# Kernel optimization log

Measured on AMD Instinct MI355X. Metric: run time of the kernel, lower is better.

The kernel has to match this reference:

```python
import jax, jax.numpy as jnp
import numpy as np
from jax import lax

B, N, D = 2, 2048, 1024
H = 16
DH = D // H
EXP = 4
INNER = EXP * D
KS = 3
POWER = 2
LN_EPS = 1e-5


def _layer_norm(x, g, b):
    mu = jnp.mean(x, axis=-1, keepdims=True)
    var = jnp.mean(jnp.square(x - mu), axis=-1, keepdims=True)
    return (x - mu) * lax.rsqrt(var + LN_EPS) * g + b


def setup_inputs() -> dict:
    key = jax.random.key(0)
    ks = jax.random.split(key, 12)
    s = 1.0 / np.sqrt(D)
    si = 1.0 / np.sqrt(INNER)
    return {
        "Q_in": jax.random.normal(ks[0], (B, N, D), jnp.float32),
        "X": jax.random.normal(ks[1], (B, N, D), jnp.float32),
        "Wq": jax.random.normal(ks[2], (D, D), jnp.float32) * s,
        "Wk": jax.random.normal(ks[3], (D, D), jnp.float32) * s,
        "Wv": jax.random.normal(ks[4], (D, D), jnp.float32) * s,
        "Wo": jax.random.normal(ks[5], (D, D), jnp.float32) * s,
        "Wup": jax.random.normal(ks[6], (D, 2 * INNER), jnp.float32) * s,
        "conv_w": jax.random.normal(ks[7], (INNER, 1, KS), jnp.float32) * 0.5,
        "Wdown": jax.random.normal(ks[8], (INNER, D), jnp.float32) * si,
        "g1": jnp.ones((D,), jnp.float32),
        "b1": jnp.zeros((D,), jnp.float32),
        "g2": jnp.ones((D,), jnp.float32),
        "b2": jnp.zeros((D,), jnp.float32),
        "dt": jnp.float32(0.1),
    }


def reference(Q_in, X, Wq, Wk, Wv, Wo, Wup, conv_w, Wdown, g1, b1, g2, b2, dt):
    Bn, Nn, d = Q_in.shape
    # --- attention path: kernelized quadratic attention (relu^power) ---
    Hc = _layer_norm(Q_in, g1, b1) + X                     # [B,N,d]
    def heads(x):
        return x.reshape(Bn, Nn, H, DH).transpose(0, 2, 1, 3)  # [B,H,N,dh]
    Qp = heads(Hc @ Wq)
    Kp = heads(Hc @ Wk)
    Vp = heads(Hc @ Wv)
    PhiQ = jax.nn.elu(Qp) + 1.0
    PhiK = jax.nn.elu(Kp) + 1.0
    W = jnp.einsum("bhnd,bhmd->bhnm", PhiQ, PhiK)          # [B,H,N,N]
    W = jnp.maximum(W, 0.0) ** POWER
    Attr = jnp.einsum("bhnm,bhmd->bhnd", W, Vp)
    Norm = jnp.sum(W, axis=-1, keepdims=True) + 1.0
    m = Attr / Norm - Vp                                   # [B,H,N,dh]
    m_concat = m.transpose(0, 2, 1, 3).reshape(Bn, Nn, d)
    dt_safe = jax.nn.softplus(dt)
    Q_interact = Q_in + dt_safe * (m_concat @ Wo)
    # --- gated depthwise-conv FFN (ConvSwiGLU) ---
    Qn2 = _layer_norm(Q_interact, g2, b2)
    GU = Qn2 @ Wup                                         # [B,N,2*INNER]
    G, U = GU[..., :INNER], GU[..., INNER:]
    Hf = jax.nn.silu(G) * U                                # [B,N,INNER]
    Hf_t = Hf.transpose(0, 2, 1)                           # [B,INNER,N]
    pad = (KS - 1) // 2
    Hc_t = lax.conv_general_dilated(
        Hf_t, conv_w, window_strides=(1,), padding=[(pad, pad)],
        dimension_numbers=("NCH", "OIH", "NCH"), feature_group_count=INNER)
    H_out = Hc_t.transpose(0, 2, 1) @ Wdown
    return Q_interact + H_out
```

## Files before the change

### kernel.cpp

```cpp
#include <hip/hip_runtime.h>

typedef unsigned short u16;
typedef __attribute__((ext_vector_type(8))) __bf16 bf16x8;
typedef __attribute__((ext_vector_type(4))) float f32x4;
typedef __attribute__((ext_vector_type(8))) unsigned short us8v;

__device__ __forceinline__ u16 f2bf(float x){
  union { float f; unsigned u; } v; v.f = x;
  unsigned r = v.u + 0x7fffu + ((v.u >> 16) & 1u);
  return (u16)(r >> 16);
}
__device__ __forceinline__ float bf2f(u16 h){
  union { unsigned u; float f; } v; v.u = ((unsigned)h) << 16;
  return v.f;
}
__device__ __forceinline__ void gld16(const void* g, void* l){
  __builtin_amdgcn_global_load_lds((const __attribute__((address_space(1))) unsigned int*)g,
                                   (__attribute__((address_space(3))) unsigned int*)l, 16, 0, 0);
}

__global__ __launch_bounds__(256) void tr_all(
    const float* __restrict__ Wq, const float* __restrict__ Wk,
    const float* __restrict__ Wv, const float* __restrict__ Wo,
    const float* __restrict__ Wup, const float* __restrict__ Wdown,
    u16* __restrict__ WqkvT, u16* __restrict__ WoT,
    u16* __restrict__ WupT, u16* __restrict__ WdT)
{
  __shared__ float t[32][33];
  int tx = threadIdx.x, ty = threadIdx.y;
  int id = blockIdx.x;
  if (id < 4096){
    int w = id >> 10, b = id & 1023;
    int c0 = (b & 31)*32, r0 = (b >> 5)*32;
    const float* S = (w==0)?Wq:(w==1)?Wk:(w==2)?Wv:Wo;
    u16* D = (w==3)? WoT : (WqkvT + (size_t)w*1024*1024);
    #pragma unroll
    for (int j=0;j<32;j+=8) t[ty+j][tx] = S[(size_t)(r0+ty+j)*1024 + (c0+tx)];
    __syncthreads();
    #pragma unroll
    for (int j=0;j<32;j+=8) D[(size_t)(c0+ty+j)*1024 + (r0+tx)] = f2bf(t[tx][ty+j]);
  } else if (id < 12288){
    int b = id - 4096;
    int c0 = (b & 255)*32, r0 = (b >> 8)*32;
    #pragma unroll
    for (int j=0;j<32;j+=8) t[ty+j][tx] = Wup[(size_t)(r0+ty+j)*8192 + (c0+tx)];
    __syncthreads();
    #pragma unroll
    for (int j=0;j<32;j+=8){
      int c = c0 + ty + j;
      int rdst = (c < 4096) ? ((c>>4)*32 + (c&15)) : (((c-4096)>>4)*32 + 16 + (c&15));
      WupT[(size_t)rdst*1024 + (r0+tx)] = f2bf(t[tx][ty+j]);
    }
  } else {
    int b = id - 12288;
    int c0 = (b & 31)*32, r0 = (b >> 5)*32;
    #pragma unroll
    for (int j=0;j<32;j+=8) t[ty+j][tx] = Wdown[(size_t)(r0+ty+j)*1024 + (c0+tx)];
    __syncthreads();
    #pragma unroll
    for (int j=0;j<32;j+=8) WdT[(size_t)(c0+ty+j)*4096 + (r0+tx)] = f2bf(t[tx][ty+j]);
  }
}

__global__ __launch_bounds__(256) void ln_kernel(const float* __restrict__ Q, const float* __restrict__ X,
    const float* __restrict__ g, const float* __restrict__ b, u16* __restrict__ O){
  int row = blockIdx.x, tid = threadIdx.x;
  const float4 x = ((const float4*)(Q + (size_t)row*1024))[tid];
  float s = x.x + x.y + x.z + x.w;
  float sq = x.x*x.x + x.y*x.y + x.z*x.z + x.w*x.w;
  #pragma unroll
  for (int o=32;o>0;o>>=1){ s += __shfl_xor(s, o); sq += __shfl_xor(sq, o); }
  __shared__ float ss[4], ssq[4];
  int wid = tid>>6;
  if ((tid&63)==0){ ss[wid]=s; ssq[wid]=sq; }
  __syncthreads();
  s = ss[0]+ss[1]+ss[2]+ss[3]; sq = ssq[0]+ssq[1]+ssq[2]+ssq[3];
  float mu = s*(1.0f/1024.0f);
  float var = sq*(1.0f/1024.0f) - mu*mu;
  float rstd = rsqrtf(var + 1e-5f);
  float4 xx = make_float4(0.f,0.f,0.f,0.f);
  if (X) xx = ((const float4*)(X + (size_t)row*1024))[tid];
  float4 gv = ((const float4*)g)[tid];
  float4 bv = ((const float4*)b)[tid];
  ushort4 o;
  o.x = f2bf((x.x-mu)*rstd*gv.x + bv.x + xx.x);
  o.y = f2bf((x.y-mu)*rstd*gv.y + bv.y + xx.y);
  o.z = f2bf((x.z-mu)*rstd*gv.z + bv.z + xx.z);
  o.w = f2bf((x.w-mu)*rstd*gv.w + bv.w + xx.w);
  ((ushort4*)(O + (size_t)row*1024))[tid] = o;
}

__global__ __launch_bounds__(256) void ln2_kernel(const float* __restrict__ P,
    const float* __restrict__ Qin, const float* __restrict__ dtp,
    const float* __restrict__ g, const float* __restrict__ b,
    float* __restrict__ Qint, u16* __restrict__ Qn2){
  int row = blockIdx.x, tid = threadIdx.x;
  float sp = log1pf(__expf(dtp[0]));
  size_t off = (size_t)row*1024;
  float4 p0 = ((const float4*)(P + off))[tid];
  float4 p1 = ((const float4*)(P + 4194304 + off))[tid];
  float4 q  = ((const float4*)(Qin + off))[tid];
  float4 x;
  x.x = q.x + sp*(p0.x+p1.x); x.y = q.y + sp*(p0.y+p1.y);
  x.z = q.z + sp*(p0.z+p1.z); x.w = q.w + sp*(p0.w+p1.w);
  ((float4*)(Qint + off))[tid] = x;
  float s = x.x + x.y + x.z + x.w;
  float sq = x.x*x.x + x.y*x.y + x.z*x.z + x.w*x.w;
  #pragma unroll
  for (int o=32;o>0;o>>=1){ s += __shfl_xor(s, o); sq += __shfl_xor(sq, o); }
  __shared__ float ss[4], ssq[4];
  int wid = tid>>6;
  if ((tid&63)==0){ ss[wid]=s; ssq[wid]=sq; }
  __syncthreads();
  s = ss[0]+ss[1]+ss[2]+ss[3]; sq = ssq[0]+ssq[1]+ssq[2]+ssq[3];
  float mu = s*(1.0f/1024.0f);
  float var = sq*(1.0f/1024.0f) - mu*mu;
  float rstd = rsqrtf(var + 1e-5f);
  float4 gv = ((const float4*)g)[tid];
  float4 bv = ((const float4*)b)[tid];
  ushort4 o;
  o.x = f2bf((x.x-mu)*rstd*gv.x + bv.x);
  o.y = f2bf((x.y-mu)*rstd*gv.y + bv.y);
  o.z = f2bf((x.z-mu)*rstd*gv.z + bv.z);
  o.w = f2bf((x.w-mu)*rstd*gv.w + bv.w);
  ((ushort4*)(Qn2 + off))[tid] = o;
}

__global__ __launch_bounds__(256, 3) void gemm_qkv(
    const u16* __restrict__ A, const u16* __restrict__ Bt, void* __restrict__ Op)
{
  __shared__ u16 As[128*32];
  __shared__ u16 Bs[128*32];
  const int tid = threadIdx.x, wid = tid>>6, lane = tid&63;
  const int g = lane>>4, l = lane&15;
  const int row0 = blockIdx.x*128, col0 = blockIdx.y*128;
  const int wr = (wid&1)*64, wc = (wid>>1)*64;
  const int l3 = l & 3;
  f32x4 acc[4][4] = {};
  for (int k0 = 0; k0 < 1024; k0 += 32){
    __syncthreads();
    #pragma unroll
    for (int i=0;i<2;i++){
      int ch0 = i*256 + wid*64;
      int ch = ch0 + lane;
      int r = ch >> 2, c = ch & 3;
      int cs = c ^ (r & 3);
      gld16(A  + (size_t)(row0+r)*1024 + k0 + cs*8, (char*)As + ch0*16);
      gld16(Bt + (size_t)(col0+r)*1024 + k0 + cs*8, (char*)Bs + ch0*16);
    }
    __syncthreads();
    bf16x8 a[4], b[4];
    #pragma unroll
    for (int i=0;i<4;i++) a[i] = *(const bf16x8*)(As + (wr + i*16 + l)*32 + (g^l3)*8);
    #pragma unroll
    for (int j=0;j<4;j++) b[j] = *(const bf16x8*)(Bs + (wc + j*16 + l)*32 + (g^l3)*8);
    #pragma unroll
    for (int i=0;i<4;i++)
      #pragma unroll
      for (int j=0;j<4;j++)
        acc[i][j] = __builtin_amdgcn_mfma_f32_16x16x32_bf16(a[i], b[j], acc[i][j], 0, 0, 0);
  }
  u16* P = (u16*)Op;
  #pragma unroll
  for (int i=0;i<4;i++)
   #pragma unroll
   for (int j=0;j<4;j++){
     int col = col0 + wc + j*16 + l;
     int qk = col >> 10, c = col & 1023;
     int h = c >> 6, d = c & 63;
     int rowb = row0 + wr + i*16 + g*4;
     int bb = rowb >> 11, n = rowb & 2047;
     if (qk == 2){
       ushort4 vs;
       vs.x = f2bf(acc[i][j][0]); vs.y = f2bf(acc[i][j][1]);
       vs.z = f2bf(acc[i][j][2]); vs.w = f2bf(acc[i][j][3]);
       *(ushort4*)(P + (size_t)8388608 + (((size_t)(bb*16 + h))*64 + d)*2048 + n) = vs;
     } else {
       #pragma unroll
       for (int r=0;r<4;r++){
         float v = acc[i][j][r];
         float phi = v > 0.f ? v + 1.f : __expf(v);
         P[(size_t)qk*4194304 + (((size_t)(bb*16 + h))*2048 + (n+r))*64 + d] = f2bf(phi);
       }
     }
   }
}

__global__ __launch_bounds__(256, 2) void gemm_wide_up(
    const u16* __restrict__ A, const u16* __restrict__ Bt, u16* __restrict__ Op)
{
  __shared__ u16 As[256*32];
  __shared__ u16 Bs[128*32];
  const int tid = threadIdx.x, wid = tid>>6, lane = tid&63;
  const int g = lane>>4, l = lane&15, l3 = l&3;
  const int bid = blockIdx.x;
  const int bx = bid & 15;
  const int by = (bid>>7)*8 + ((bid>>4) & 7);
  const int row0 = bx*256, col0 = by*128;
  const int wr = (wid&1)*128, wc = (wid>>1)*64;
  f32x4 acc[8][4] = {};
  for (int k0 = 0; k0 < 1024; k0 += 32){
    __syncthreads();
    #pragma unroll
    for (int i=0;i<4;i++){
      int ch0 = i*256 + wid*64;
      int ch = ch0 + lane;
      int r = ch >> 2, c = ch & 3;
      int cs = c ^ (r & 3);
      gld16(A + (size_t)(row0+r)*1024 + k0 + cs*8, (char*)As + ch0*16);
    }
    #pragma unroll
    for (int i=0;i<2;i++){
      int ch0 = i*256 + wid*64;
      int ch = ch0 + lane;
      int r = ch >> 2, c = ch & 3;
      int cs = c ^ (r & 3);
      gld16(Bt + (size_t)(col0+r)*1024 + k0 + cs*8, (char*)Bs + ch0*16);
    }
    __syncthreads();
    bf16x8 a[8], b[4];
    #pragma unroll
    for (int i=0;i<8;i++) a[i] = *(const bf16x8*)(As + (wr + i*16 + l)*32 + (g^l3)*8);
    #pragma unroll
    for (int j=0;j<4;j++) b[j] = *(const bf16x8*)(Bs + (wc + j*16 + l)*32 + (g^l3)*8);
    #pragma unroll
    for (int i=0;i<8;i++)
      #pragma unroll
      for (int j=0;j<4;j++)
        acc[i][j] = __builtin_amdgcn_mfma_f32_16x16x32_bf16(a[i], b[j], acc[i][j], 0, 0, 0);
  }
  #pragma unroll
  for (int i=0;i<8;i++)
   #pragma unroll
   for (int jj=0;jj<4;jj+=2)
    #pragma unroll
    for (int r=0;r<4;r++){
      int row = row0 + wr + i*16 + g*4 + r;
      int pair = (col0 + wc + jj*16) >> 5;
      float G = acc[i][jj][r], U = acc[i][jj+1][r];
      float hf = G/(1.f+__expf(-G))*U;
      Op[(size_t)row*4096 + pair*16 + l] = f2bf(hf);
    }
}

__global__ __launch_bounds__(256, 3) void gemm_part(
    const u16* __restrict__ A, const u16* __restrict__ Bt,
    int Nc, int K, int Ks, float* __restrict__ Op)
{
  __shared__ u16 As[128*32];
  __shared__ u16 Bs[128*32];
  const int tid = threadIdx.x, wid = tid>>6, lane = tid&63;
  const int g = lane>>4, l = lane&15;
  const int row0 = blockIdx.x*128, col0 = blockIdx.y*128;
  const int kbase = blockIdx.z*Ks;
  const int wr = (wid&1)*64, wc = (wid>>1)*64;
  const int l3 = l & 3;
  f32x4 acc[4][4] = {};
  for (int k0 = kbase; k0 < kbase + Ks; k0 += 32){
    __syncthreads();
    #pragma unroll
    for (int i=0;i<2;i++){
      int ch0 = i*256 + wid*64;
      int ch = ch0 + lane;
      int r = ch >> 2, c = ch & 3;
      int cs = c ^ (r & 3);
      gld16(A  + (size_t)(row0+r)*K + k0 + cs*8, (char*)As + ch0*16);
      gld16(Bt + (size_t)(col0+r)*K + k0 + cs*8, (char*)Bs + ch0*16);
    }
    __syncthreads();
    bf16x8 a[4], b[4];
    #pragma unroll
    for (int i=0;i<4;i++) a[i] = *(const bf16x8*)(As + (wr + i*16 + l)*32 + (g^l3)*8);
    #pragma unroll
    for (int j=0;j<4;j++) b[j] = *(const bf16x8*)(Bs + (wc + j*16 + l)*32 + (g^l3)*8);
    #pragma unroll
    for (int i=0;i<4;i++)
      #pragma unroll
      for (int j=0;j<4;j++)
        acc[i][j] = __builtin_amdgcn_mfma_f32_16x16x32_bf16(a[i], b[j], acc[i][j], 0, 0, 0);
  }
  float* P = Op + (size_t)blockIdx.z*4194304;
  #pragma unroll
  for (int i=0;i<4;i++)
   #pragma unroll
   for (int j=0;j<4;j++)
    #pragma unroll
    for (int r=0;r<4;r++){
      int row = row0 + wr + i*16 + g*4 + r;
      int col = col0 + wc + j*16 + l;
      P[(size_t)row*Nc + col] = acc[i][j][r];
    }
}

__global__ __launch_bounds__(256) void reduce_out(const float* __restrict__ Qint,
    const float* __restrict__ P, float* __restrict__ out){
  size_t i = (size_t)blockIdx.x*256 + threadIdx.x;
  float4 a  = ((const float4*)Qint)[i];
  float4 p0 = ((const float4*)P)[i];
  float4 p1 = ((const float4*)(P + 4194304))[i];
  float4 o;
  o.x = a.x + p0.x + p1.x; o.y = a.y + p0.y + p1.y;
  o.z = a.z + p0.z + p1.z; o.w = a.w + p0.w + p1.w;
  ((float4*)out)[i] = o;
}

__global__ __launch_bounds__(256, 2) void attn_kernel(
    const u16* __restrict__ PhiQ, const u16* __restrict__ PhiK,
    const u16* __restrict__ Vt, u16* __restrict__ Mb)
{
  __shared__ u16 sK[2][128][32];
  __shared__ u16 sV[4][64][32];
  __shared__ u16 sW[128*128];
  const int tid = threadIdx.x, wid = tid>>6, lane = tid&63;
  const int g = lane>>4, l = lane&15;
  const int l3 = l & 3;
  const int q0 = blockIdx.x*128, bh = blockIdx.y;
  const u16* Q  = PhiQ + (size_t)bh*2048*64;
  const u16* Kb = PhiK + (size_t)bh*2048*64;
  const u16* V  = Vt   + (size_t)bh*64*2048;
  bf16x8 bq[8][2];
  #pragma unroll
  for (int ct=0;ct<8;ct++)
    #pragma unroll
    for (int ks=0;ks<2;ks++)
      bq[ct][ks] = *(const bf16x8*)(Q + (size_t)(q0 + ct*16 + l)*64 + ks*32 + g*8);
  f32x4 accO[2][4] = {};
  float rsum[8] = {0.f,0.f,0.f,0.f,0.f,0.f,0.f,0.f};
  for (int m0 = 0; m0 < 2048; m0 += 128){
    __syncthreads();
    #pragma unroll
    for (int ks=0; ks<2; ks++)
      #pragma unroll
      for (int i=0;i<2;i++){
        int ch0 = i*256 + wid*64;
        int ch = ch0 + lane;
        int r = ch >> 2, q = ch & 3;
        int qs = q ^ (r & 3);
        gld16(Kb + (size_t)(m0+r)*64 + ks*32 + qs*8, (char*)&sK[ks][0][0] + ch0*16);
      }
    #pragma unroll
    for (int c=0; c<4; c++){
      int ch0 = wid*64;
      int ch = ch0 + lane;
      int d = ch >> 2, q = ch & 3;
      int qs = q ^ (d & 3);
      gld16(V + (size_t)d*2048 + m0 + c*32 + qs*8, (char*)&sV[c][0][0] + ch0*16);
    }
    __syncthreads();
    f32x4 st[2][8] = {};
    bf16x8 ak[2][2];
    #pragma unroll
    for (int rt=0;rt<2;rt++)
      #pragma unroll
      for (int ks=0;ks<2;ks++)
        ak[rt][ks] = *(const bf16x8*)&sK[ks][wid*32 + rt*16 + l][(g^l3)*8];
    #pragma unroll
    for (int ct=0;ct<8;ct++){
      #pragma unroll
      for (int ks=0;ks<2;ks++){
        st[0][ct] = __builtin_amdgcn_mfma_f32_16x16x32_bf16(ak[0][ks], bq[ct][ks], st[0][ct], 0,0,0);
        st[1][ct] = __builtin_amdgcn_mfma_f32_16x16x32_bf16(ak[1][ks], bq[ct][ks], st[1][ct], 0,0,0);
      }
    }
    #pragma unroll
    for (int ct=0;ct<8;ct++){
      float part = 0.f;
      #pragma unroll
      for (int rt=0;rt<2;rt++){
        float s0 = fmaxf(st[rt][ct][0], 0.f), s1 = fmaxf(st[rt][ct][1], 0.f);
        float s2 = fmaxf(st[rt][ct][2], 0.f), s3 = fmaxf(st[rt][ct][3], 0.f);
        float w0 = s0*s0, w1 = s1*s1, w2 = s2*s2, w3 = s3*s3;
        part += w0 + w1 + w2 + w3;
        int n = ct*16 + l;
        int mblk = wid*4 + rt*2 + (g>>1);
        ushort4 w4;
        w4.x = f2bf(w0); w4.y = f2bf(w1); w4.z = f2bf(w2); w4.w = f2bf(w3);
        *(ushort4*)(sW + n*128 + ((mblk ^ l)*8) + (g&1)*4) = w4;
      }
      rsum[ct] += part;
    }
    __syncthreads();
    #pragma unroll
    for (int ks=0;ks<4;ks++){
      int n0 = wid*32 + l, n1 = wid*32 + 16 + l;
      bf16x8 aw0 = *(const bf16x8*)(sW + n0*128 + (((ks*4+g) ^ (n0&15))*8));
      bf16x8 aw1 = *(const bf16x8*)(sW + n1*128 + (((ks*4+g) ^ (n1&15))*8));
      #pragma unroll
      for (int ct=0;ct<4;ct++){
        bf16x8 bv = *(const bf16x8*)&sV[ks][ct*16 + l][(g^l3)*8];
        accO[0][ct] = __builtin_amdgcn_mfma_f32_16x16x32_bf16(aw0, bv, accO[0][ct], 0,0,0);
        accO[1][ct] = __builtin_amdgcn_mfma_f32_16x16x32_bf16(aw1, bv, accO[1][ct], 0,0,0);
      }
    }
  }
  __syncthreads();
  float* sRS = (float*)sW;
  float* sNorm = ((float*)sW) + 512;
  #pragma unroll
  for (int ct=0;ct<8;ct++){
    float v = rsum[ct];
    v += __shfl_xor(v, 16);
    v += __shfl_xor(v, 32);
    rsum[ct] = v;
  }
  if (g == 0){
    #pragma unroll
    for (int ct=0;ct<8;ct++) sRS[wid*128 + ct*16 + l] = rsum[ct];
  }
  __syncthreads();
  if (tid < 128) sNorm[tid] = sRS[tid] + sRS[128+tid] + sRS[256+tid] + sRS[384+tid] + 1.0f;
  __syncthreads();
  const int bb = bh >> 4, h = bh & 15;
  #pragma unroll
  for (int rt=0;rt<2;rt++)
   #pragma unroll
   for (int ct=0;ct<4;ct++)
    #pragma unroll
    for (int r=0;r<4;r++){
      int n = wid*32 + rt*16 + g*4 + r;
      int d = ct*16 + l;
      float norm = sNorm[n];
      float vv = bf2f(V[(size_t)d*2048 + q0 + n]);
      float mv = accO[rt][ct][r]/norm - vv;
      Mb[((size_t)(bb*2048) + q0 + n)*1024 + h*64 + d] = f2bf(mv);
    }
}

__global__ __launch_bounds__(256) void conv_kernel(const u16* __restrict__ Hf, const float* __restrict__ w,
                                                   u16* __restrict__ Cv){
  int row = blockIdx.y;
  int n = row & 2047;
  int c0 = (blockIdx.x*256 + threadIdx.x)*8;
  us8v h0 = {0,0,0,0,0,0,0,0}, h2 = {0,0,0,0,0,0,0,0};
  us8v h1 = *(const us8v*)(Hf + (size_t)row*4096 + c0);
  if (n > 0)    h0 = *(const us8v*)(Hf + (size_t)(row-1)*4096 + c0);
  if (n < 2047) h2 = *(const us8v*)(Hf + (size_t)(row+1)*4096 + c0);
  us8v o;
  #pragma unroll
  for (int e=0;e<8;e++){
    int c = c0 + e;
    float acc = bf2f(h0[e])*w[c*3+0] + bf2f(h1[e])*w[c*3+1] + bf2f(h2[e])*w[c*3+2];
    o[e] = f2bf(acc);
  }
  *(us8v*)(Cv + (size_t)row*4096 + c0) = o;
}

extern "C" void kernel_launch(void* const* d_in, const int* in_sizes, int n_in,
                              void* d_out, int out_size, void* d_ws, size_t ws_size,
                              hipStream_t stream)
{
  const float* Q_in  = (const float*)d_in[0];
  const float* X     = (const float*)d_in[1];
  const float* Wq    = (const float*)d_in[2];
  const float* Wk    = (const float*)d_in[3];
  const float* Wv    = (const float*)d_in[4];
  const float* Wo    = (const float*)d_in[5];
  const float* Wup   = (const float*)d_in[6];
  const float* convw = (const float*)d_in[7];
  const float* Wdown = (const float*)d_in[8];
  const float* g1    = (const float*)d_in[9];
  const float* b1    = (const float*)d_in[10];
  const float* g2    = (const float*)d_in[11];
  const float* b2    = (const float*)d_in[12];
  const float* dt    = (const float*)d_in[13];
  float* out = (float*)d_out;

  char* ws = (char*)d_ws;
  const size_t MB = (size_t)1 << 20;
  u16* HcB   = (u16*)(ws + 0*MB);
  u16* WqkvT = (u16*)(ws + 8*MB);
  u16* WoT   = (u16*)(ws + 14*MB);
  u16* PhiQ  = (u16*)(ws + 16*MB);
  u16* Vt    = (u16*)(ws + 32*MB);
  u16* Mb    = (u16*)(ws + 40*MB);
  float* Po  = (float*)(ws + 48*MB);
  u16* WupT  = (u16*)(ws + 80*MB);
  u16* WdT   = (u16*)(ws + 96*MB);
  float* Qint = (float*)(ws + 104*MB);
  u16* Qn2   = (u16*)(ws + 120*MB);
  u16* Hf    = (u16*)(ws + 0*MB);
  u16* Cv    = (u16*)(ws + 40*MB);
  float* Pd  = (float*)(ws + 0*MB);
  u16* PhiK  = PhiQ + 4194304;

  tr_all<<<16384, dim3(32, 8), 0, stream>>>(Wq, Wk, Wv, Wo, Wup, Wdown,
                                            WqkvT, WoT, WupT, WdT);

  ln_kernel<<<4096, 256, 0, stream>>>(Q_in, X, g1, b1, HcB);

  gemm_qkv<<<dim3(32, 24), 256, 0, stream>>>(HcB, WqkvT, PhiQ);

  attn_kernel<<<dim3(16, 32), 256, 0, stream>>>(PhiQ, PhiK, Vt, Mb);

  gemm_part<<<dim3(32, 8, 2), 256, 0, stream>>>(Mb, WoT, 1024, 1024, 512, Po);

  ln2_kernel<<<4096, 256, 0, stream>>>(Po, Q_in, dt, g2, b2, Qint, Qn2);

  gemm_wide_up<<<1024, 256, 0, stream>>>(Qn2, WupT, Hf);

  conv_kernel<<<dim3(2, 4096), 256, 0, stream>>>(Hf, convw, Cv);

  gemm_part<<<dim3(32, 8, 2), 256, 0, stream>>>(Cv, WdT, 1024, 4096, 2048, Pd);
  reduce_out<<<4096, 256, 0, stream>>>(Qint, Pd, out);
}
```

Baseline: 434.4 us.

## Widen GEMM K-tile to 64, store split-K partials in bf16, fuse LN1 into transpose

```diff
diff --git a/kernel.cpp b/kernel.cpp
--- a/kernel.cpp
+++ b/kernel.cpp
@@ -24,11 +24,40 @@
     const float* __restrict__ Wv, const float* __restrict__ Wo,
     const float* __restrict__ Wup, const float* __restrict__ Wdown,
     u16* __restrict__ WqkvT, u16* __restrict__ WoT,
-    u16* __restrict__ WupT, u16* __restrict__ WdT)
+    u16* __restrict__ WupT, u16* __restrict__ WdT,
+    const float* __restrict__ Qin, const float* __restrict__ X,
+    const float* __restrict__ g1, const float* __restrict__ b1,
+    u16* __restrict__ HcB)
 {
   __shared__ float t[32][33];
   int tx = threadIdx.x, ty = threadIdx.y;
   int id = blockIdx.x;
+  if (id >= 16384){
+    int row = id - 16384, tid = ty*32 + tx;
+    const float4 x = ((const float4*)(Qin + (size_t)row*1024))[tid];
+    float s = x.x + x.y + x.z + x.w;
+    float sq = x.x*x.x + x.y*x.y + x.z*x.z + x.w*x.w;
+    #pragma unroll
+    for (int o=32;o>0;o>>=1){ s += __shfl_xor(s, o); sq += __shfl_xor(sq, o); }
+    __shared__ float ss[4], ssq[4];
+    int wid = tid>>6;
+    if ((tid&63)==0){ ss[wid]=s; ssq[wid]=sq; }
+    __syncthreads();
+    s = ss[0]+ss[1]+ss[2]+ss[3]; sq = ssq[0]+ssq[1]+ssq[2]+ssq[3];
+    float mu = s*(1.0f/1024.0f);
+    float var = sq*(1.0f/1024.0f) - mu*mu;
+    float rstd = rsqrtf(var + 1e-5f);
+    float4 xx = ((const float4*)(X + (size_t)row*1024))[tid];
+    float4 gv = ((const float4*)g1)[tid];
+    float4 bv = ((const float4*)b1)[tid];
+    ushort4 o;
+    o.x = f2bf((x.x-mu)*rstd*gv.x + bv.x + xx.x);
+    o.y = f2bf((x.y-mu)*rstd*gv.y + bv.y + xx.y);
+    o.z = f2bf((x.z-mu)*rstd*gv.z + bv.z + xx.z);
+    o.w = f2bf((x.w-mu)*rstd*gv.w + bv.w + xx.w);
+    ((ushort4*)(HcB + (size_t)row*1024))[tid] = o;
+    return;
+  }
   if (id < 4096){
     int w = id >> 10, b = id & 1023;
     int c0 = (b & 31)*32, r0 = (b >> 5)*32;
@@ -62,47 +91,19 @@
   }
 }
 
-__global__ __launch_bounds__(256) void ln_kernel(const float* __restrict__ Q, const float* __restrict__ X,
-    const float* __restrict__ g, const float* __restrict__ b, u16* __restrict__ O){
-  int row = blockIdx.x, tid = threadIdx.x;
-  const float4 x = ((const float4*)(Q + (size_t)row*1024))[tid];
-  float s = x.x + x.y + x.z + x.w;
-  float sq = x.x*x.x + x.y*x.y + x.z*x.z + x.w*x.w;
-  #pragma unroll
-  for (int o=32;o>0;o>>=1){ s += __shfl_xor(s, o); sq += __shfl_xor(sq, o); }
-  __shared__ float ss[4], ssq[4];
-  int wid = tid>>6;
-  if ((tid&63)==0){ ss[wid]=s; ssq[wid]=sq; }
-  __syncthreads();
-  s = ss[0]+ss[1]+ss[2]+ss[3]; sq = ssq[0]+ssq[1]+ssq[2]+ssq[3];
-  float mu = s*(1.0f/1024.0f);
-  float var = sq*(1.0f/1024.0f) - mu*mu;
-  float rstd = rsqrtf(var + 1e-5f);
-  float4 xx = make_float4(0.f,0.f,0.f,0.f);
-  if (X) xx = ((const float4*)(X + (size_t)row*1024))[tid];
-  float4 gv = ((const float4*)g)[tid];
-  float4 bv = ((const float4*)b)[tid];
-  ushort4 o;
-  o.x = f2bf((x.x-mu)*rstd*gv.x + bv.x + xx.x);
-  o.y = f2bf((x.y-mu)*rstd*gv.y + bv.y + xx.y);
-  o.z = f2bf((x.z-mu)*rstd*gv.z + bv.z + xx.z);
-  o.w = f2bf((x.w-mu)*rstd*gv.w + bv.w + xx.w);
-  ((ushort4*)(O + (size_t)row*1024))[tid] = o;
-}
-
-__global__ __launch_bounds__(256) void ln2_kernel(const float* __restrict__ P,
+__global__ __launch_bounds__(256) void ln2_kernel(const u16* __restrict__ P,
     const float* __restrict__ Qin, const float* __restrict__ dtp,
     const float* __restrict__ g, const float* __restrict__ b,
     float* __restrict__ Qint, u16* __restrict__ Qn2){
   int row = blockIdx.x, tid = threadIdx.x;
   float sp = log1pf(__expf(dtp[0]));
   size_t off = (size_t)row*1024;
-  float4 p0 = ((const float4*)(P + off))[tid];
-  float4 p1 = ((const float4*)(P + 4194304 + off))[tid];
+  ushort4 p0 = ((const ushort4*)(P + off))[tid];
+  ushort4 p1 = ((const ushort4*)(P + 4194304 + off))[tid];
   float4 q  = ((const float4*)(Qin + off))[tid];
   float4 x;
-  x.x = q.x + sp*(p0.x+p1.x); x.y = q.y + sp*(p0.y+p1.y);
-  x.z = q.z + sp*(p0.z+p1.z); x.w = q.w + sp*(p0.w+p1.w);
+  x.x = q.x + sp*(bf2f(p0.x)+bf2f(p1.x)); x.y = q.y + sp*(bf2f(p0.y)+bf2f(p1.y));
+  x.z = q.z + sp*(bf2f(p0.z)+bf2f(p1.z)); x.w = q.w + sp*(bf2f(p0.w)+bf2f(p1.w));
   ((float4*)(Qint + off))[tid] = x;
   float s = x.x + x.y + x.z + x.w;
   float sq = x.x*x.x + x.y*x.y + x.z*x.z + x.w*x.w;
@@ -129,36 +130,38 @@
 __global__ __launch_bounds__(256, 3) void gemm_qkv(
     const u16* __restrict__ A, const u16* __restrict__ Bt, void* __restrict__ Op)
 {
-  __shared__ u16 As[128*32];
-  __shared__ u16 Bs[128*32];
+  __shared__ u16 As[128*64];
+  __shared__ u16 Bs[128*64];
   const int tid = threadIdx.x, wid = tid>>6, lane = tid&63;
-  const int g = lane>>4, l = lane&15;
+  const int g = lane>>4, l = lane&15, l7 = l&7;
   const int row0 = blockIdx.x*128, col0 = blockIdx.y*128;
   const int wr = (wid&1)*64, wc = (wid>>1)*64;
-  const int l3 = l & 3;
   f32x4 acc[4][4] = {};
-  for (int k0 = 0; k0 < 1024; k0 += 32){
-    __syncthreads();
-    #pragma unroll
-    for (int i=0;i<2;i++){
+  for (int k0 = 0; k0 < 1024; k0 += 64){
+    __syncthreads();
+    #pragma unroll
+    for (int i=0;i<4;i++){
       int ch0 = i*256 + wid*64;
       int ch = ch0 + lane;
-      int r = ch >> 2, c = ch & 3;
-      int cs = c ^ (r & 3);
+      int r = ch >> 3, c = ch & 7;
+      int cs = c ^ (r & 7);
       gld16(A  + (size_t)(row0+r)*1024 + k0 + cs*8, (char*)As + ch0*16);
       gld16(Bt + (size_t)(col0+r)*1024 + k0 + cs*8, (char*)Bs + ch0*16);
     }
     __syncthreads();
-    bf16x8 a[4], b[4];
-    #pragma unroll
-    for (int i=0;i<4;i++) a[i] = *(const bf16x8*)(As + (wr + i*16 + l)*32 + (g^l3)*8);
-    #pragma unroll
-    for (int j=0;j<4;j++) b[j] = *(const bf16x8*)(Bs + (wc + j*16 + l)*32 + (g^l3)*8);
-    #pragma unroll
-    for (int i=0;i<4;i++)
-      #pragma unroll
-      for (int j=0;j<4;j++)
-        acc[i][j] = __builtin_amdgcn_mfma_f32_16x16x32_bf16(a[i], b[j], acc[i][j], 0, 0, 0);
+    #pragma unroll
+    for (int kk=0; kk<2; kk++){
+      bf16x8 a[4], b[4];
+      #pragma unroll
+      for (int i=0;i<4;i++) a[i] = *(const bf16x8*)(As + (wr + i*16 + l)*64 + (((kk*4+g)^l7)*8));
+      #pragma unroll
+      for (int j=0;j<4;j++) b[j] = *(const bf16x8*)(Bs + (wc + j*16 + l)*64 + (((kk*4+g)^l7)*8));
+      #pragma unroll
+      for (int i=0;i<4;i++)
+        #pragma unroll
+        for (int j=0;j<4;j++)
+          acc[i][j] = __builtin_amdgcn_mfma_f32_16x16x32_bf16(a[i], b[j], acc[i][j], 0, 0, 0);
+    }
   }
   u16* P = (u16*)Op;
   #pragma unroll
@@ -189,45 +192,48 @@
 __global__ __launch_bounds__(256, 2) void gemm_wide_up(
     const u16* __restrict__ A, const u16* __restrict__ Bt, u16* __restrict__ Op)
 {
-  __shared__ u16 As[256*32];
-  __shared__ u16 Bs[128*32];
+  __shared__ u16 As[256*64];
+  __shared__ u16 Bs[128*64];
   const int tid = threadIdx.x, wid = tid>>6, lane = tid&63;
-  const int g = lane>>4, l = lane&15, l3 = l&3;
+  const int g = lane>>4, l = lane&15, l7 = l&7;
   const int bid = blockIdx.x;
   const int bx = bid & 15;
   const int by = (bid>>7)*8 + ((bid>>4) & 7);
   const int row0 = bx*256, col0 = by*128;
   const int wr = (wid&1)*128, wc = (wid>>1)*64;
   f32x4 acc[8][4] = {};
-  for (int k0 = 0; k0 < 1024; k0 += 32){
-    __syncthreads();
+  for (int k0 = 0; k0 < 1024; k0 += 64){
+    __syncthreads();
+    #pragma unroll
+    for (int i=0;i<8;i++){
+      int ch0 = i*256 + wid*64;
+      int ch = ch0 + lane;
+      int r = ch >> 3, c = ch & 7;
+      int cs = c ^ (r & 7);
+      gld16(A + (size_t)(row0+r)*1024 + k0 + cs*8, (char*)As + ch0*16);
+    }
     #pragma unroll
     for (int i=0;i<4;i++){
       int ch0 = i*256 + wid*64;
       int ch = ch0 + lane;
-      int r = ch >> 2, c = ch & 3;
-      int cs = c ^ (r & 3);
-      gld16(A + (size_t)(row0+r)*1024 + k0 + cs*8, (char*)As + ch0*16);
-    }
-    #pragma unroll
-    for (int i=0;i<2;i++){
-      int ch0 = i*256 + wid*64;
-      int ch = ch0 + lane;
-      int r = ch >> 2, c = ch & 3;
-      int cs = c ^ (r & 3);
+      int r = ch >> 3, c = ch & 7;
+      int cs = c ^ (r & 7);
       gld16(Bt + (size_t)(col0+r)*1024 + k0 + cs*8, (char*)Bs + ch0*16);
     }
     __syncthreads();
-    bf16x8 a[8], b[4];
-    #pragma unroll
-    for (int i=0;i<8;i++) a[i] = *(const bf16x8*)(As + (wr + i*16 + l)*32 + (g^l3)*8);
-    #pragma unroll
-    for (int j=0;j<4;j++) b[j] = *(const bf16x8*)(Bs + (wc + j*16 + l)*32 + (g^l3)*8);
-    #pragma unroll
-    for (int i=0;i<8;i++)
-      #pragma unroll
-      for (int j=0;j<4;j++)
-        acc[i][j] = __builtin_amdgcn_mfma_f32_16x16x32_bf16(a[i], b[j], acc[i][j], 0, 0, 0);
+    #pragma unroll
+    for (int kk=0; kk<2; kk++){
+      bf16x8 a[8], b[4];
+      #pragma unroll
+      for (int i=0;i<8;i++) a[i] = *(const bf16x8*)(As + (wr + i*16 + l)*64 + (((kk*4+g)^l7)*8));
+      #pragma unroll
+      for (int j=0;j<4;j++) b[j] = *(const bf16x8*)(Bs + (wc + j*16 + l)*64 + (((kk*4+g)^l7)*8));
+      #pragma unroll
+      for (int i=0;i<8;i++)
+        #pragma unroll
+        for (int j=0;j<4;j++)
+          acc[i][j] = __builtin_amdgcn_mfma_f32_16x16x32_bf16(a[i], b[j], acc[i][j], 0, 0, 0);
+    }
   }
   #pragma unroll
   for (int i=0;i<8;i++)
@@ -245,41 +251,43 @@
 
 __global__ __launch_bounds__(256, 3) void gemm_part(
     const u16* __restrict__ A, const u16* __restrict__ Bt,
-    int Nc, int K, int Ks, float* __restrict__ Op)
+    int Nc, int K, int Ks, u16* __restrict__ Op)
 {
-  __shared__ u16 As[128*32];
-  __shared__ u16 Bs[128*32];
+  __shared__ u16 As[128*64];
+  __shared__ u16 Bs[128*64];
   const int tid = threadIdx.x, wid = tid>>6, lane = tid&63;
-  const int g = lane>>4, l = lane&15;
+  const int g = lane>>4, l = lane&15, l7 = l&7;
   const int row0 = blockIdx.x*128, col0 = blockIdx.y*128;
   const int kbase = blockIdx.z*Ks;
   const int wr = (wid&1)*64, wc = (wid>>1)*64;
-  const int l3 = l & 3;
   f32x4 acc[4][4] = {};
-  for (int k0 = kbase; k0 < kbase + Ks; k0 += 32){
-    __syncthreads();
-    #pragma unroll
-    for (int i=0;i<2;i++){
+  for (int k0 = kbase; k0 < kbase + Ks; k0 += 64){
+    __syncthreads();
+    #pragma unroll
+    for (int i=0;i<4;i++){
       int ch0 = i*256 + wid*64;
       int ch = ch0 + lane;
-      int r = ch >> 2, c = ch & 3;
-      int cs = c ^ (r & 3);
+      int r = ch >> 3, c = ch & 7;
+      int cs = c ^ (r & 7);
       gld16(A  + (size_t)(row0+r)*K + k0 + cs*8, (char*)As + ch0*16);
       gld16(Bt + (size_t)(col0+r)*K + k0 + cs*8, (char*)Bs + ch0*16);
     }
     __syncthreads();
-    bf16x8 a[4], b[4];
-    #pragma unroll
-    for (int i=0;i<4;i++) a[i] = *(const bf16x8*)(As + (wr + i*16 + l)*32 + (g^l3)*8);
-    #pragma unroll
-    for (int j=0;j<4;j++) b[j] = *(const bf16x8*)(Bs + (wc + j*16 + l)*32 + (g^l3)*8);
-    #pragma unroll
-    for (int i=0;i<4;i++)
-      #pragma unroll
-      for (int j=0;j<4;j++)
-        acc[i][j] = __builtin_amdgcn_mfma_f32_16x16x32_bf16(a[i], b[j], acc[i][j], 0, 0, 0);
-  }
-  float* P = Op + (size_t)blockIdx.z*4194304;
+    #pragma unroll
+    for (int kk=0; kk<2; kk++){
+      bf16x8 a[4], b[4];
+      #pragma unroll
+      for (int i=0;i<4;i++) a[i] = *(const bf16x8*)(As + (wr + i*16 + l)*64 + (((kk*4+g)^l7)*8));
+      #pragma unroll
+      for (int j=0;j<4;j++) b[j] = *(const bf16x8*)(Bs + (wc + j*16 + l)*64 + (((kk*4+g)^l7)*8));
+      #pragma unroll
+      for (int i=0;i<4;i++)
+        #pragma unroll
+        for (int j=0;j<4;j++)
+          acc[i][j] = __builtin_amdgcn_mfma_f32_16x16x32_bf16(a[i], b[j], acc[i][j], 0, 0, 0);
+    }
+  }
+  u16* P = Op + (size_t)blockIdx.z*4194304;
   #pragma unroll
   for (int i=0;i<4;i++)
    #pragma unroll
@@ -288,19 +296,19 @@
     for (int r=0;r<4;r++){
       int row = row0 + wr + i*16 + g*4 + r;
       int col = col0 + wc + j*16 + l;
-      P[(size_t)row*Nc + col] = acc[i][j][r];
+      P[(size_t)row*Nc + col] = f2bf(acc[i][j][r]);
     }
 }
 
 __global__ __launch_bounds__(256) void reduce_out(const float* __restrict__ Qint,
-    const float* __restrict__ P, float* __restrict__ out){
+    const u16* __restrict__ P, float* __restrict__ out){
   size_t i = (size_t)blockIdx.x*256 + threadIdx.x;
   float4 a  = ((const float4*)Qint)[i];
-  float4 p0 = ((const float4*)P)[i];
-  float4 p1 = ((const float4*)(P + 4194304))[i];
+  ushort4 p0 = ((const ushort4*)P)[i];
+  ushort4 p1 = ((const ushort4*)(P + 4194304))[i];
   float4 o;
-  o.x = a.x + p0.x + p1.x; o.y = a.y + p0.y + p1.y;
-  o.z = a.z + p0.z + p1.z; o.w = a.w + p0.w + p1.w;
+  o.x = a.x + bf2f(p0.x) + bf2f(p1.x); o.y = a.y + bf2f(p0.y) + bf2f(p1.y);
+  o.z = a.z + bf2f(p0.z) + bf2f(p1.z); o.w = a.w + bf2f(p0.w) + bf2f(p1.w);
   ((float4*)out)[i] = o;
 }
 
@@ -473,20 +481,19 @@
   u16* PhiQ  = (u16*)(ws + 16*MB);
   u16* Vt    = (u16*)(ws + 32*MB);
   u16* Mb    = (u16*)(ws + 40*MB);
-  float* Po  = (float*)(ws + 48*MB);
+  u16* Po    = (u16*)(ws + 48*MB);
   u16* WupT  = (u16*)(ws + 80*MB);
   u16* WdT   = (u16*)(ws + 96*MB);
   float* Qint = (float*)(ws + 104*MB);
   u16* Qn2   = (u16*)(ws + 120*MB);
   u16* Hf    = (u16*)(ws + 0*MB);
   u16* Cv    = (u16*)(ws + 40*MB);
-  float* Pd  = (float*)(ws + 0*MB);
+  u16* Pd    = (u16*)(ws + 0*MB);
   u16* PhiK  = PhiQ + 4194304;
 
-  tr_all<<<16384, dim3(32, 8), 0, stream>>>(Wq, Wk, Wv, Wo, Wup, Wdown,
-                                            WqkvT, WoT, WupT, WdT);
-
-  ln_kernel<<<4096, 256, 0, stream>>>(Q_in, X, g1, b1, HcB);
+  tr_all<<<20480, dim3(32, 8), 0, stream>>>(Wq, Wk, Wv, Wo, Wup, Wdown,
+                                            WqkvT, WoT, WupT, WdT,
+                                            Q_in, X, g1, b1, HcB);
 
   gemm_qkv<<<dim3(32, 24), 256, 0, stream>>>(HcB, WqkvT, PhiQ);
 
```

Measured after the change: 389.2 us. 1.12x faster.
